# Performance work log

Hardware: AMD Instinct MI355X
Metric: run time of the kernel (lower is better)

## Reference

```python
import jax, jax.numpy as jnp
import numpy as np

N_NODES = 50000
D_FEAT = 512
H1, H2 = 128, 64
N_CLASSES = 40
E_MP = 800000
E_LP = 250000


def gcn_conv(x, W, b, edge_index, edge_weight, num_nodes):
    """PyG GCNConv: add self-loops, symmetric norm D^-1/2 (A+I) D^-1/2, then (norm-agg)(xW)+b."""
    row, col = edge_index[0], edge_index[1]
    loop = jnp.arange(num_nodes)
    row = jnp.concatenate([row, loop])
    col = jnp.concatenate([col, loop])
    ew = jnp.concatenate([edge_weight, jnp.ones((num_nodes,), x.dtype)])
    deg = jax.ops.segment_sum(ew, col, num_segments=num_nodes)
    dinv = jnp.where(deg > 0, deg ** -0.5, 0.0).astype(x.dtype)
    norm = dinv[row] * ew * dinv[col]  # [E+N]
    h = x @ W  # [N, out]
    msg = h[row] * norm[:, None]  # gather + scale per edge
    out = jax.ops.segment_sum(msg, col, num_segments=num_nodes) + b
    return out


def setup_inputs() -> dict:
    key = jax.random.key(0)
    ks = jax.random.split(key, 16)
    inp = {}
    inp["x"] = jax.random.normal(ks[0], (N_NODES, D_FEAT), jnp.float32)
    inp["train_pos_edge_index"] = jax.random.randint(ks[1], (2, E_MP), 0, N_NODES)
    inp["edge_index"] = jax.random.randint(ks[2], (2, E_MP), 0, N_NODES)
    inp["edge_weight"] = jax.random.uniform(ks[3], (E_MP,), jnp.float32)
    inp["pos_edge_index"] = jax.random.randint(ks[4], (2, E_LP), 0, N_NODES)
    inp["neg_edge_index"] = jax.random.randint(ks[5], (2, E_LP), 0, N_NODES)
    # parameters (glorot-ish scaled)
    def w(k, i, o):
        return jax.random.normal(k, (i, o), jnp.float32) * (2.0 / (i + o)) ** 0.5
    inp["W1"] = w(ks[6], D_FEAT, H1)
    inp["b1"] = jnp.zeros((H1,), jnp.float32)
    inp["W2"] = w(ks[7], H1, H2)
    inp["b2"] = jnp.zeros((H2,), jnp.float32)
    inp["W_attr"] = w(ks[8], H2, N_CLASSES)
    inp["b_attr"] = jnp.zeros((N_CLASSES,), jnp.float32)
    inp["W_att"] = w(ks[9], H2, N_CLASSES)
    inp["b_att"] = jnp.zeros((N_CLASSES,), jnp.float32)
    return inp


def reference(x, train_pos_edge_index, edge_index, edge_weight, pos_edge_index,
              neg_edge_index, W1, b1, W2, b2, W_attr, b_attr, W_att, b_att):
    ones = jnp.ones((train_pos_edge_index.shape[1],), x.dtype)
    h = jax.nn.relu(gcn_conv(x, W1, b1, train_pos_edge_index, ones, N_NODES))
    h = gcn_conv(h, W2, b2, train_pos_edge_index, ones, N_NODES)  # [N, 64]
    attr = gcn_conv(h, W_attr, b_attr, edge_index, edge_weight, N_NODES)
    # gradient reversal is identity in forward
    att = gcn_conv(h, W_att, b_att, edge_index, edge_weight, N_NODES)
    total = jnp.concatenate([pos_edge_index, neg_edge_index], axis=-1)  # [2, 2*E_LP]
    x_j = h[total[0]]
    x_i = h[total[1]]
    res = jnp.einsum("ef,ef->e", x_i, x_j)
    return res, jax.nn.log_softmax(attr, axis=1), jax.nn.log_softmax(att, axis=1)
```

## Files before the change

### kernel.cpp

```cpp
#include <hip/hip_runtime.h>

typedef short s16x8 __attribute__((ext_vector_type(8)));
typedef short s16x4 __attribute__((ext_vector_type(4)));
typedef float f32x4 __attribute__((ext_vector_type(4)));

static __device__ __forceinline__ unsigned short f2bf(float f) {
  unsigned u = __float_as_uint(f);
  u += 0x7fff + ((u >> 16) & 1);
  return (unsigned short)(u >> 16);
}
static __device__ __forceinline__ float bf2f(unsigned short h) {
  return __uint_as_float(((unsigned)h) << 16);
}


static __global__ void k_init(int* cntT, int* cntE, int n) {
  int i = blockIdx.x * blockDim.x + threadIdx.x;
  if (i < n) { cntT[i] = 0; cntE[i] = 0; }
}

static __global__ void k_count(const int* __restrict__ tcol, const int* __restrict__ ecol,
                               int* __restrict__ cntT, int* __restrict__ cntE,
                               int* __restrict__ rankT, int* __restrict__ rankE, int E) {
  int e = blockIdx.x * blockDim.x + threadIdx.x;
  if (e < E) {
    rankT[e] = atomicAdd(&cntT[tcol[e]], 1);
    rankE[e] = atomicAdd(&cntE[ecol[e]], 1);
  }
}

static __global__ __launch_bounds__(256) void k_scanA(
    const int* __restrict__ cntT, const int* __restrict__ cntE,
    int* __restrict__ bsum, int n, int nb) {
  const int* cnt = blockIdx.y ? cntE : cntT;
  int tid = threadIdx.x;
  int base = blockIdx.x * 1024 + tid * 4;
  int s = 0;
#pragma unroll
  for (int q = 0; q < 4; ++q) { int i = base + q; if (i < n) s += cnt[i]; }
  __shared__ int red[256];
  red[tid] = s;
  __syncthreads();
  for (int off = 128; off > 0; off >>= 1) {
    if (tid < off) red[tid] += red[tid + off];
    __syncthreads();
  }
  if (tid == 0) bsum[blockIdx.y * nb + blockIdx.x] = red[0];
}

static __global__ void k_scanB(int* bsum, int* ptrT, int* ptrE, int nb, int n) {
  int a = threadIdx.x;
  if (a > 1) return;
  int* bs = bsum + a * nb;
  int run = 0;
  for (int i = 0; i < nb; ++i) { int c = bs[i]; bs[i] = run; run += c; }
  (a ? ptrE : ptrT)[n] = run;
}

static __global__ __launch_bounds__(256) void k_scanC(
    const int* __restrict__ cntT, const int* __restrict__ cntE,
    const int* __restrict__ bsum, int* __restrict__ ptrT, int* __restrict__ ptrE,
    int n, int nb) {
  const int* cnt = blockIdx.y ? cntE : cntT;
  int* ptr = blockIdx.y ? ptrE : ptrT;
  int tid = threadIdx.x;
  int pre = bsum[blockIdx.y * nb + blockIdx.x];
  int base = blockIdx.x * 1024 + tid * 4;
  int v[4];
  int s = 0;
#pragma unroll
  for (int q = 0; q < 4; ++q) { int i = base + q; v[q] = (i < n) ? cnt[i] : 0; s += v[q]; }
  __shared__ int red[256];
  red[tid] = s;
  __syncthreads();
  for (int off = 1; off < 256; off <<= 1) {
    int t = (tid >= off) ? red[tid - off] : 0;
    __syncthreads();
    red[tid] += t;
    __syncthreads();
  }
  int run = pre + (tid ? red[tid - 1] : 0);
#pragma unroll
  for (int q = 0; q < 4; ++q) {
    int i = base + q;
    if (i < n) ptr[i] = run;
    run += v[q];
  }
}

static __global__ void k_fill(const int* __restrict__ trow, const int* __restrict__ tcol,
                              const int* __restrict__ erow, const int* __restrict__ ecol,
                              const float* __restrict__ ew,
                              const int* __restrict__ ptrT, const int* __restrict__ ptrE,
                              const int* __restrict__ rankT, const int* __restrict__ rankE,
                              int* __restrict__ srcT, int2* __restrict__ srcwE, int E) {
  int e = blockIdx.x * blockDim.x + threadIdx.x;
  if (e >= E) return;
  srcT[ptrT[tcol[e]] + rankT[e]] = trow[e];
  int2 p;
  p.x = erow[e];
  p.y = __float_as_int(ew[e]);
  srcwE[ptrE[ecol[e]] + rankE[e]] = p;
}

static __global__ void k_dinv2(const int* __restrict__ cntT, const int2* __restrict__ srcwE,
                               const int* __restrict__ ptrE,
                               float* __restrict__ dinvT, float* __restrict__ dinvE, int n) {
  int i = blockIdx.x * blockDim.x + threadIdx.x;
  if (i >= n) return;
  dinvT[i] = rsqrtf((float)cntT[i] + 1.0f);
  float s = 1.0f;
  int e = ptrE[i + 1];
  for (int j = ptrE[i]; j < e; ++j) s += __int_as_float(srcwE[j].y);
  dinvE[i] = rsqrtf(s);
}


static __global__ void k_cvtW(const float* __restrict__ W, unsigned short* __restrict__ Wh,
                              unsigned short* __restrict__ Wl, int K, int Nc) {
  int t = blockIdx.x * blockDim.x + threadIdx.x;
  if (t >= K * Nc) return;
  int k = t / Nc, c = t - k * Nc;
  float v = W[t];
  unsigned short hi = f2bf(v);
  Wh[(size_t)c * K + k] = hi;
  Wl[(size_t)c * K + k] = f2bf(v - bf2f(hi));
}


#define PADU 36

static __global__ __launch_bounds__(256) void k_gemm_mfma_split(
    const float* __restrict__ A, const unsigned short* __restrict__ Bh,
    const unsigned short* __restrict__ Bl, float* __restrict__ C, int M, int K) {
  __shared__ __align__(16) unsigned short Ah[64][PADU];
  __shared__ __align__(16) unsigned short Al[64][PADU];
  int tid = threadIdx.x;
  int lane = tid & 63, wid = tid >> 6;
  int wr = wid >> 1, wc = wid & 1;
  int l15 = lane & 15, l4 = lane >> 4;
  int brow = blockIdx.x * 64;
  f32x4 acc[2][4] = {};

  float4 v[2];
#pragma unroll
  for (int q = 0; q < 2; ++q) {
    int idx = tid + q * 256;
    int r = idx >> 3, c4 = (idx & 7) * 4;
    int gr = brow + r;
    v[q] = (gr < M) ? *(const float4*)&A[(size_t)gr * K + c4]
                    : make_float4(0.f, 0.f, 0.f, 0.f);
  }

  for (int k0 = 0; k0 < K; k0 += 32) {
    __syncthreads();
#pragma unroll
    for (int q = 0; q < 2; ++q) {
      int idx = tid + q * 256;
      int r = idx >> 3, c4 = (idx & 7) * 4;
      float4 w = v[q];
      unsigned short h0 = f2bf(w.x), h1 = f2bf(w.y), h2 = f2bf(w.z), h3 = f2bf(w.w);
      s16x4 hv = {(short)h0, (short)h1, (short)h2, (short)h3};
      s16x4 lv = {(short)f2bf(w.x - bf2f(h0)), (short)f2bf(w.y - bf2f(h1)),
                  (short)f2bf(w.z - bf2f(h2)), (short)f2bf(w.w - bf2f(h3))};
      *(s16x4*)&Ah[r][c4] = hv;
      *(s16x4*)&Al[r][c4] = lv;
    }
    if (k0 + 32 < K) {
#pragma unroll
      for (int q = 0; q < 2; ++q) {
        int idx = tid + q * 256;
        int r = idx >> 3, c4 = (idx & 7) * 4;
        int gr = brow + r;
        v[q] = (gr < M) ? *(const float4*)&A[(size_t)gr * K + k0 + 32 + c4]
                        : make_float4(0.f, 0.f, 0.f, 0.f);
      }
    }
    __syncthreads();

    s16x8 afh[2], afl[2];
#pragma unroll
    for (int m = 0; m < 2; ++m) {
      int r = wr * 32 + m * 16 + l15;
      afh[m] = *(const s16x8*)&Ah[r][l4 * 8];
      afl[m] = *(const s16x8*)&Al[r][l4 * 8];
    }
    s16x8 bfh[4], bfl[4];
#pragma unroll
    for (int n = 0; n < 4; ++n) {
      int c = wc * 64 + n * 16 + l15;
      bfh[n] = *(const s16x8*)&Bh[(size_t)c * K + k0 + l4 * 8];
      bfl[n] = *(const s16x8*)&Bl[(size_t)c * K + k0 + l4 * 8];
    }
#pragma unroll
    for (int m = 0; m < 2; ++m)
#pragma unroll
      for (int n = 0; n < 4; ++n) {
        acc[m][n] = __builtin_amdgcn_mfma_f32_16x16x32_bf16(afh[m], bfh[n], acc[m][n], 0, 0, 0);
        acc[m][n] = __builtin_amdgcn_mfma_f32_16x16x32_bf16(afl[m], bfh[n], acc[m][n], 0, 0, 0);
        acc[m][n] = __builtin_amdgcn_mfma_f32_16x16x32_bf16(afh[m], bfl[n], acc[m][n], 0, 0, 0);
      }
  }
#pragma unroll
  for (int m = 0; m < 2; ++m) {
    int rbase = brow + wr * 32 + m * 16 + l4 * 4;
#pragma unroll
    for (int n = 0; n < 4; ++n) {
      int c = wc * 64 + n * 16 + l15;
#pragma unroll
      for (int j = 0; j < 4; ++j) {
        int r = rbase + j;
        if (r < M) C[(size_t)r * 128 + c] = acc[m][n][j];
      }
    }
  }
}


template <int F, bool RELU, bool WEIGHTED>
static __global__ __launch_bounds__(256) void k_gather4(
    const float* __restrict__ H, const int* __restrict__ rowptr,
    const int* __restrict__ src, const int2* __restrict__ srcw,
    const float* __restrict__ dinv, const float* __restrict__ Hpre,
    const float* __restrict__ bias, float* __restrict__ out, int n) {
  const int L = F / 4;
  int node = blockIdx.x * (256 / L) + threadIdx.x / L;
  if (node >= n) return;
  int f4 = (threadIdx.x % L) * 4;
  float d = dinv[node];
  float4 hp = *(const float4*)&Hpre[(size_t)node * F + f4];
  float ax = hp.x * d, ay = hp.y * d, az = hp.z * d, aw = hp.w * d;
  int j = rowptr[node], e = rowptr[node + 1];
  for (; j + 1 < e; j += 2) {
    int r0, r1;
    float w0, w1;
    if (WEIGHTED) {
      int2 a = srcw[j], b = srcw[j + 1];
      r0 = a.x; r1 = b.x;
      w0 = dinv[r0] * __int_as_float(a.y);
      w1 = dinv[r1] * __int_as_float(b.y);
    } else {
      r0 = src[j]; r1 = src[j + 1];
      w0 = dinv[r0]; w1 = dinv[r1];
    }
    float4 v0 = *(const float4*)&H[(size_t)r0 * F + f4];
    float4 v1 = *(const float4*)&H[(size_t)r1 * F + f4];
    ax += v0.x * w0 + v1.x * w1;
    ay += v0.y * w0 + v1.y * w1;
    az += v0.z * w0 + v1.z * w1;
    aw += v0.w * w0 + v1.w * w1;
  }
  if (j < e) {
    int r;
    float wj;
    if (WEIGHTED) { int2 a = srcw[j]; r = a.x; wj = dinv[r] * __int_as_float(a.y); }
    else { r = src[j]; wj = dinv[r]; }
    float4 v = *(const float4*)&H[(size_t)r * F + f4];
    ax += v.x * wj; ay += v.y * wj; az += v.z * wj; aw += v.w * wj;
  }
  float bx = 0, by = 0, bz = 0, bw = 0;
  if (bias) { float4 bb = *(const float4*)&bias[f4]; bx = bb.x; by = bb.y; bz = bb.z; bw = bb.w; }
  ax = ax * d + bx; ay = ay * d + by; az = az * d + bz; aw = aw * d + bw;
  if (RELU) { ax = fmaxf(ax, 0.f); ay = fmaxf(ay, 0.f); az = fmaxf(az, 0.f); aw = fmaxf(aw, 0.f); }
  float4 o; o.x = ax; o.y = ay; o.z = az; o.w = aw;
  *(float4*)&out[(size_t)node * F + f4] = o;
}


static __global__ __launch_bounds__(256) void k_gemm(
    const float* __restrict__ A, const float* __restrict__ B,
    const float* __restrict__ bias, float* __restrict__ C,
    int M, int N, int K) {
  const int BM = 64, BN = 64, BK = 16;
  __shared__ float As[BK][BM + 4];
  __shared__ float Bs[BK][BN + 4];
  int tid = threadIdx.x;
  int tr = tid >> 4, tc = tid & 15;
  int brow = blockIdx.y * BM, bcol = blockIdx.x * BN;
  float acc[4][4] = {};
  for (int k0 = 0; k0 < K; k0 += BK) {
#pragma unroll
    for (int i = tid; i < BM * BK; i += 256) {
      int m = i >> 4, kk = i & 15;
      int gr = brow + m;
      As[kk][m] = (gr < M) ? A[(size_t)gr * K + k0 + kk] : 0.f;
    }
#pragma unroll
    for (int i = tid; i < BK * BN; i += 256) {
      int kk = i >> 6, n = i & 63;
      int gc = bcol + n;
      Bs[kk][n] = (gc < N) ? B[(size_t)(k0 + kk) * N + gc] : 0.f;
    }
    __syncthreads();
#pragma unroll
    for (int kk = 0; kk < BK; ++kk) {
      float a[4], b[4];
#pragma unroll
      for (int i = 0; i < 4; ++i) a[i] = As[kk][tr * 4 + i];
#pragma unroll
      for (int j = 0; j < 4; ++j) b[j] = Bs[kk][tc * 4 + j];
#pragma unroll
      for (int i = 0; i < 4; ++i)
#pragma unroll
        for (int j = 0; j < 4; ++j) acc[i][j] += a[i] * b[j];
    }
    __syncthreads();
  }
#pragma unroll
  for (int i = 0; i < 4; ++i) {
    int r = brow + tr * 4 + i;
    if (r >= M) continue;
#pragma unroll
    for (int j = 0; j < 4; ++j) {
      int c = bcol + tc * 4 + j;
      if (c < N) C[(size_t)r * N + c] = acc[i][j] + (bias ? bias[c] : 0.f);
    }
  }
}


static __global__ void k_logsoftmax40(float* __restrict__ X, int n) {
  int i = blockIdx.x * blockDim.x + threadIdx.x;
  if (i >= n) return;
  float4 v[10];
#pragma unroll
  for (int q = 0; q < 10; ++q) v[q] = *(const float4*)&X[(size_t)i * 40 + q * 4];
  float m = -1e30f;
#pragma unroll
  for (int q = 0; q < 10; ++q)
    m = fmaxf(m, fmaxf(fmaxf(v[q].x, v[q].y), fmaxf(v[q].z, v[q].w)));
  float s = 0.f;
#pragma unroll
  for (int q = 0; q < 10; ++q)
    s += expf(v[q].x - m) + expf(v[q].y - m) + expf(v[q].z - m) + expf(v[q].w - m);
  float ls = logf(s) + m;
#pragma unroll
  for (int q = 0; q < 10; ++q) {
    float4 o; o.x = v[q].x - ls; o.y = v[q].y - ls; o.z = v[q].z - ls; o.w = v[q].w - ls;
    *(float4*)&X[(size_t)i * 40 + q * 4] = o;
  }
}


static __global__ __launch_bounds__(256) void k_linkpred4(
    const float* __restrict__ H2, const int* __restrict__ pos,
    const int* __restrict__ neg, float* __restrict__ res, int Elp) {
  int t = blockIdx.x * 256 + threadIdx.x;
  int e = t >> 4, f4 = (t & 15) * 4;
  if (e >= 2 * Elp) return;
  int a, b;
  if (e < Elp) { a = pos[e]; b = pos[Elp + e]; }
  else { int e2 = e - Elp; a = neg[e2]; b = neg[Elp + e2]; }
  float4 va = *(const float4*)&H2[(size_t)a * 64 + f4];
  float4 vb = *(const float4*)&H2[(size_t)b * 64 + f4];
  float p = va.x * vb.x + va.y * vb.y + va.z * vb.z + va.w * vb.w;
  p += __shfl_xor(p, 1);
  p += __shfl_xor(p, 2);
  p += __shfl_xor(p, 4);
  p += __shfl_xor(p, 8);
  if ((t & 15) == 0) res[e] = p;
}


extern "C" void kernel_launch(void* const* d_in, const int* in_sizes, int n_in,
                              void* d_out, int out_size, void* d_ws, size_t ws_size,
                              hipStream_t stream) {
  const float* x    = (const float*)d_in[0];
  const int*   tp   = (const int*)d_in[1];
  const int*   ei   = (const int*)d_in[2];
  const float* ew   = (const float*)d_in[3];
  const int*   pos  = (const int*)d_in[4];
  const int*   neg  = (const int*)d_in[5];
  const float* W1   = (const float*)d_in[6];
  const float* b1   = (const float*)d_in[7];
  const float* W2   = (const float*)d_in[8];
  const float* b2   = (const float*)d_in[9];
  const float* Wattr= (const float*)d_in[10];
  const float* battr= (const float*)d_in[11];
  const float* Watt = (const float*)d_in[12];
  const float* batt = (const float*)d_in[13];

  const int N   = in_sizes[0] / 512;
  const int EMP = in_sizes[1] / 2;
  const int ELP = in_sizes[4] / 2;
  const int NB  = (N + 1023) / 1024;

  float* ws = (float*)d_ws;
  float* dinvT = ws;
  float* dinvE = dinvT + N;
  int* rowptrT = (int*)(dinvE + N);
  int* rowptrE = rowptrT + (N + 4);
  int* srcT    = rowptrE + (N + 4);
  int2* srcwE  = (int2*)(srcT + EMP);
  int* bsum    = (int*)(srcwE + EMP);
  unsigned short* W1h = (unsigned short*)(bsum + 128);
  unsigned short* W1l = W1h + 512 * 128;
  float* bufA  = (float*)(W1l + 512 * 128);
  float* bufB  = bufA + (size_t)N * 128;
  float* bufC  = bufB + (size_t)N * 128;
  int* rankT = (int*)bufA;
  int* rankE = rankT + EMP;
  int* cntT  = (int*)bufB;
  int* cntE  = cntT + N;

  float* out_res  = (float*)d_out;
  float* out_attr = out_res + 2 * (size_t)ELP;
  float* out_att  = out_attr + (size_t)N * 40;

  dim3 b256(256);
  int gN = (N + 255) / 256;
  int gE = (EMP + 255) / 256;

  k_init<<<gN, b256, 0, stream>>>(cntT, cntE, N);
  k_cvtW<<<(512 * 128 + 255) / 256, b256, 0, stream>>>(W1, W1h, W1l, 512, 128);
  k_count<<<gE, b256, 0, stream>>>(tp + EMP, ei + EMP, cntT, cntE, rankT, rankE, EMP);
  {
    dim3 gs(NB, 2);
    k_scanA<<<gs, b256, 0, stream>>>(cntT, cntE, bsum, N, NB);
    k_scanB<<<1, 64, 0, stream>>>(bsum, rowptrT, rowptrE, NB, N);
    k_scanC<<<gs, b256, 0, stream>>>(cntT, cntE, bsum, rowptrT, rowptrE, N, NB);
  }
  k_fill<<<gE, b256, 0, stream>>>(tp, tp + EMP, ei, ei + EMP, ew,
                                  rowptrT, rowptrE, rankT, rankE, srcT, srcwE, EMP);
  k_dinv2<<<gN, b256, 0, stream>>>(cntT, srcwE, rowptrE, dinvT, dinvE, N);

  k_gemm_mfma_split<<<(N + 63) / 64, b256, 0, stream>>>(x, W1h, W1l, bufA, N, 512);
  k_gather4<128, true, false><<<(N + 7) / 8, b256, 0, stream>>>(
      bufA, rowptrT, srcT, nullptr, dinvT, bufA, b1, bufB, N);

  {
    dim3 grid(1, (N + 63) / 64);
    k_gemm<<<grid, b256, 0, stream>>>(bufB, W2, nullptr, bufA, N, 64, 128);
  }
  k_gather4<64, false, false><<<(N + 15) / 16, b256, 0, stream>>>(
      bufA, rowptrT, srcT, nullptr, dinvT, bufA, b2, bufC, N);

  k_gather4<64, false, true><<<(N + 15) / 16, b256, 0, stream>>>(
      bufC, rowptrE, nullptr, srcwE, dinvE, bufC, nullptr, bufA, N);

  {
    dim3 grid(1, (N + 63) / 64);
    k_gemm<<<grid, b256, 0, stream>>>(bufA, Wattr, battr, out_attr, N, 40, 64);
    k_gemm<<<grid, b256, 0, stream>>>(bufA, Watt, batt, out_att, N, 40, 64);
  }
  k_logsoftmax40<<<gN, b256, 0, stream>>>(out_attr, N);
  k_logsoftmax40<<<gN, b256, 0, stream>>>(out_att, N);

  k_linkpred4<<<(2 * ELP * 16 + 255) / 256, b256, 0, stream>>>(bufC, pos, neg, out_res, ELP);
}
```

Measured before the change: 455.6 us.

## Tile W into K-major 32-wide blocks and software-pipeline GEMM B loads

The split-bf16 weight is now stored in 32-element K tiles so each k-step's B fragment sits in one contiguous 8KB chunk. The GEMM main loop is restructured to prefetch the next tile's A rows and B fragments into registers before issuing the current tile's MFMAs, so global load latency overlaps compute. The cost is more live registers for the double-buffered B fragments, which could lower occupancy. The fixed 4096 stride per k-tile assumes 128 output columns.

```diff
diff --git a/kernel.cpp b/kernel.cpp
--- a/kernel.cpp
+++ b/kernel.cpp
@@ -123,8 +123,9 @@
   int k = t / Nc, c = t - k * Nc;
   float v = W[t];
   unsigned short hi = f2bf(v);
-  Wh[(size_t)c * K + k] = hi;
-  Wl[(size_t)c * K + k] = f2bf(v - bf2f(hi));
+  size_t o = (size_t)(k >> 5) * (Nc * 32) + c * 32 + (k & 31);
+  Wh[o] = hi;
+  Wl[o] = f2bf(v - bf2f(hi));
 }
 
 
@@ -140,9 +141,13 @@
   int wr = wid >> 1, wc = wid & 1;
   int l15 = lane & 15, l4 = lane >> 4;
   int brow = blockIdx.x * 64;
+  const int NKT = K >> 5;
   f32x4 acc[2][4] = {};
 
   float4 v[2];
+  s16x8 bhc[4], blc[4], bhn[4], bln[4];
+  s16x8 afh[2], afl[2];
+
 #pragma unroll
   for (int q = 0; q < 2; ++q) {
     int idx = tid + q * 256;
@@ -151,8 +156,60 @@
     v[q] = (gr < M) ? *(const float4*)&A[(size_t)gr * K + c4]
                     : make_float4(0.f, 0.f, 0.f, 0.f);
   }
-
-  for (int k0 = 0; k0 < K; k0 += 32) {
+#pragma unroll
+  for (int n = 0; n < 4; ++n) {
+    size_t o = (size_t)(wc * 64 + n * 16 + l15) * 32 + l4 * 8;
+    bhc[n] = *(const s16x8*)&Bh[o];
+    blc[n] = *(const s16x8*)&Bl[o];
+  }
+#pragma unroll
+  for (int q = 0; q < 2; ++q) {
+    int idx = tid + q * 256;
+    int r = idx >> 3, c4 = (idx & 7) * 4;
+    float4 w = v[q];
+    unsigned short h0 = f2bf(w.x), h1 = f2bf(w.y), h2 = f2bf(w.z), h3 = f2bf(w.w);
+    s16x4 hv = {(short)h0, (short)h1, (short)h2, (short)h3};
+    s16x4 lv = {(short)f2bf(w.x - bf2f(h0)), (short)f2bf(w.y - bf2f(h1)),
+                (short)f2bf(w.z - bf2f(h2)), (short)f2bf(w.w - bf2f(h3))};
+    *(s16x4*)&Ah[r][c4] = hv;
+    *(s16x4*)&Al[r][c4] = lv;
+  }
+  __syncthreads();
+#pragma unroll
+  for (int m = 0; m < 2; ++m) {
+    int r = wr * 32 + m * 16 + l15;
+    afh[m] = *(const s16x8*)&Ah[r][l4 * 8];
+    afl[m] = *(const s16x8*)&Al[r][l4 * 8];
+  }
+
+  for (int kt = 0;; ++kt) {
+    bool more = (kt + 1 < NKT);
+    if (more) {
+      int k0 = (kt + 1) * 32;
+#pragma unroll
+      for (int q = 0; q < 2; ++q) {
+        int idx = tid + q * 256;
+        int r = idx >> 3, c4 = (idx & 7) * 4;
+        int gr = brow + r;
+        v[q] = (gr < M) ? *(const float4*)&A[(size_t)gr * K + k0 + c4]
+                        : make_float4(0.f, 0.f, 0.f, 0.f);
+      }
+#pragma unroll
+      for (int n = 0; n < 4; ++n) {
+        size_t o = (size_t)(kt + 1) * 4096 + (size_t)(wc * 64 + n * 16 + l15) * 32 + l4 * 8;
+        bhn[n] = *(const s16x8*)&Bh[o];
+        bln[n] = *(const s16x8*)&Bl[o];
+      }
+    }
+#pragma unroll
+    for (int m = 0; m < 2; ++m)
+#pragma unroll
+      for (int n = 0; n < 4; ++n) {
+        acc[m][n] = __builtin_amdgcn_mfma_f32_16x16x32_bf16(afh[m], bhc[n], acc[m][n], 0, 0, 0);
+        acc[m][n] = __builtin_amdgcn_mfma_f32_16x16x32_bf16(afl[m], bhc[n], acc[m][n], 0, 0, 0);
+        acc[m][n] = __builtin_amdgcn_mfma_f32_16x16x32_bf16(afh[m], blc[n], acc[m][n], 0, 0, 0);
+      }
+    if (!more) break;
     __syncthreads();
 #pragma unroll
     for (int q = 0; q < 2; ++q) {
@@ -166,41 +223,17 @@
       *(s16x4*)&Ah[r][c4] = hv;
       *(s16x4*)&Al[r][c4] = lv;
     }
-    if (k0 + 32 < K) {
-#pragma unroll
-      for (int q = 0; q < 2; ++q) {
-        int idx = tid + q * 256;
-        int r = idx >> 3, c4 = (idx & 7) * 4;
-        int gr = brow + r;
-        v[q] = (gr < M) ? *(const float4*)&A[(size_t)gr * K + k0 + 32 + c4]
-                        : make_float4(0.f, 0.f, 0.f, 0.f);
-      }
-    }
-    __syncthreads();
-
-    s16x8 afh[2], afl[2];
+    __syncthreads();
 #pragma unroll
     for (int m = 0; m < 2; ++m) {
       int r = wr * 32 + m * 16 + l15;
       afh[m] = *(const s16x8*)&Ah[r][l4 * 8];
       afl[m] = *(const s16x8*)&Al[r][l4 * 8];
     }
-    s16x8 bfh[4], bfl[4];
-#pragma unroll
-    for (int n = 0; n < 4; ++n) {
-      int c = wc * 64 + n * 16 + l15;
-      bfh[n] = *(const s16x8*)&Bh[(size_t)c * K + k0 + l4 * 8];
-      bfl[n] = *(const s16x8*)&Bl[(size_t)c * K + k0 + l4 * 8];
-    }
-#pragma unroll
-    for (int m = 0; m < 2; ++m)
-#pragma unroll
-      for (int n = 0; n < 4; ++n) {
-        acc[m][n] = __builtin_amdgcn_mfma_f32_16x16x32_bf16(afh[m], bfh[n], acc[m][n], 0, 0, 0);
-        acc[m][n] = __builtin_amdgcn_mfma_f32_16x16x32_bf16(afl[m], bfh[n], acc[m][n], 0, 0, 0);
-        acc[m][n] = __builtin_amdgcn_mfma_f32_16x16x32_bf16(afh[m], bfl[n], acc[m][n], 0, 0, 0);
-      }
-  }
+#pragma unroll
+    for (int n = 0; n < 4; ++n) { bhc[n] = bhn[n]; blc[n] = bln[n]; }
+  }
+
 #pragma unroll
   for (int m = 0; m < 2; ++m) {
     int rbase = brow + wr * 32 + m * 16 + l4 * 4;
```

New measurement: 435.0 us. 4.5% less time.

## Double-buffer split-bf16 GEMM, tile W layout, vectorize edge count/fill

Applied to the files above, without the earlier changes.

The first-layer GEMM now double-buffers the A tile in shared memory, prefetches B fragments one k-step ahead in registers, and uses one barrier per k-step. The k-loop is fully unrolled for a fixed K of 512. The converted W1 is stored in a k-tiled layout so each lane's B fragment loads are contiguous, and the edge count and fill kernels each handle four edges per thread with int4 loads. The aim is to hide global load latency behind MFMA work and cut load instruction count, at the cost of more registers and shared memory and of hardcoding K.

```diff
diff --git a/kernel.cpp b/kernel.cpp
--- a/kernel.cpp
+++ b/kernel.cpp
@@ -22,10 +22,26 @@
 static __global__ void k_count(const int* __restrict__ tcol, const int* __restrict__ ecol,
                                int* __restrict__ cntT, int* __restrict__ cntE,
                                int* __restrict__ rankT, int* __restrict__ rankE, int E) {
-  int e = blockIdx.x * blockDim.x + threadIdx.x;
-  if (e < E) {
-    rankT[e] = atomicAdd(&cntT[tcol[e]], 1);
-    rankE[e] = atomicAdd(&cntE[ecol[e]], 1);
+  int base = (blockIdx.x * blockDim.x + threadIdx.x) * 4;
+  if (base + 3 < E) {
+    int4 tc = *(const int4*)&tcol[base];
+    int4 ec = *(const int4*)&ecol[base];
+    int4 rt, re;
+    rt.x = atomicAdd(&cntT[tc.x], 1);
+    rt.y = atomicAdd(&cntT[tc.y], 1);
+    rt.z = atomicAdd(&cntT[tc.z], 1);
+    rt.w = atomicAdd(&cntT[tc.w], 1);
+    re.x = atomicAdd(&cntE[ec.x], 1);
+    re.y = atomicAdd(&cntE[ec.y], 1);
+    re.z = atomicAdd(&cntE[ec.z], 1);
+    re.w = atomicAdd(&cntE[ec.w], 1);
+    *(int4*)&rankT[base] = rt;
+    *(int4*)&rankE[base] = re;
+  } else {
+    for (int e = base; e < E; ++e) {
+      rankT[e] = atomicAdd(&cntT[tcol[e]], 1);
+      rankE[e] = atomicAdd(&cntE[ecol[e]], 1);
+    }
   }
 }
 
@@ -94,13 +110,33 @@
                               const int* __restrict__ ptrT, const int* __restrict__ ptrE,
                               const int* __restrict__ rankT, const int* __restrict__ rankE,
                               int* __restrict__ srcT, int2* __restrict__ srcwE, int E) {
-  int e = blockIdx.x * blockDim.x + threadIdx.x;
-  if (e >= E) return;
-  srcT[ptrT[tcol[e]] + rankT[e]] = trow[e];
-  int2 p;
-  p.x = erow[e];
-  p.y = __float_as_int(ew[e]);
-  srcwE[ptrE[ecol[e]] + rankE[e]] = p;
+  int base = (blockIdx.x * blockDim.x + threadIdx.x) * 4;
+  if (base + 3 < E) {
+    int4 tr = *(const int4*)&trow[base];
+    int4 tc = *(const int4*)&tcol[base];
+    int4 er = *(const int4*)&erow[base];
+    int4 ec = *(const int4*)&ecol[base];
+    float4 w = *(const float4*)&ew[base];
+    int4 rt = *(const int4*)&rankT[base];
+    int4 re = *(const int4*)&rankE[base];
+    srcT[ptrT[tc.x] + rt.x] = tr.x;
+    srcT[ptrT[tc.y] + rt.y] = tr.y;
+    srcT[ptrT[tc.z] + rt.z] = tr.z;
+    srcT[ptrT[tc.w] + rt.w] = tr.w;
+    int2 p;
+    p.x = er.x; p.y = __float_as_int(w.x); srcwE[ptrE[ec.x] + re.x] = p;
+    p.x = er.y; p.y = __float_as_int(w.y); srcwE[ptrE[ec.y] + re.y] = p;
+    p.x = er.z; p.y = __float_as_int(w.z); srcwE[ptrE[ec.z] + re.z] = p;
+    p.x = er.w; p.y = __float_as_int(w.w); srcwE[ptrE[ec.w] + re.w] = p;
+  } else {
+    for (int e = base; e < E; ++e) {
+      srcT[ptrT[tcol[e]] + rankT[e]] = trow[e];
+      int2 p;
+      p.x = erow[e];
+      p.y = __float_as_int(ew[e]);
+      srcwE[ptrE[ecol[e]] + rankE[e]] = p;
+    }
+  }
 }
 
 static __global__ void k_dinv2(const int* __restrict__ cntT, const int2* __restrict__ srcwE,
@@ -123,18 +159,21 @@
   int k = t / Nc, c = t - k * Nc;
   float v = W[t];
   unsigned short hi = f2bf(v);
-  Wh[(size_t)c * K + k] = hi;
-  Wl[(size_t)c * K + k] = f2bf(v - bf2f(hi));
+  size_t o = (size_t)(k >> 5) * (Nc * 32) + c * 32 + (k & 31);
+  Wh[o] = hi;
+  Wl[o] = f2bf(v - bf2f(hi));
 }
 
 
 #define PADU 36
+#define GK 512
+#define NKT 16
 
 static __global__ __launch_bounds__(256) void k_gemm_mfma_split(
     const float* __restrict__ A, const unsigned short* __restrict__ Bh,
-    const unsigned short* __restrict__ Bl, float* __restrict__ C, int M, int K) {
-  __shared__ __align__(16) unsigned short Ah[64][PADU];
-  __shared__ __align__(16) unsigned short Al[64][PADU];
+    const unsigned short* __restrict__ Bl, float* __restrict__ C, int M) {
+  __shared__ __align__(16) unsigned short Ah[2][64][PADU];
+  __shared__ __align__(16) unsigned short Al[2][64][PADU];
   int tid = threadIdx.x;
   int lane = tid & 63, wid = tid >> 6;
   int wr = wid >> 1, wc = wid & 1;
@@ -142,65 +181,103 @@
   int brow = blockIdx.x * 64;
   f32x4 acc[2][4] = {};
 
+  int ar = tid >> 3, ac4 = (tid & 7) * 4;
+  int ar2 = (tid + 256) >> 3, ac42 = ((tid + 256) & 7) * 4;
+  const float* Arow1 = &A[(size_t)min(brow + ar, M - 1) * GK + ac4];
+  const float* Arow2 = &A[(size_t)min(brow + ar2, M - 1) * GK + ac42];
+  bool v1ok = (brow + ar < M), v2ok = (brow + ar2 < M);
+
   float4 v[2];
-#pragma unroll
-  for (int q = 0; q < 2; ++q) {
-    int idx = tid + q * 256;
-    int r = idx >> 3, c4 = (idx & 7) * 4;
-    int gr = brow + r;
-    v[q] = (gr < M) ? *(const float4*)&A[(size_t)gr * K + c4]
-                    : make_float4(0.f, 0.f, 0.f, 0.f);
-  }
-
-  for (int k0 = 0; k0 < K; k0 += 32) {
-    __syncthreads();
-#pragma unroll
-    for (int q = 0; q < 2; ++q) {
-      int idx = tid + q * 256;
-      int r = idx >> 3, c4 = (idx & 7) * 4;
-      float4 w = v[q];
-      unsigned short h0 = f2bf(w.x), h1 = f2bf(w.y), h2 = f2bf(w.z), h3 = f2bf(w.w);
-      s16x4 hv = {(short)h0, (short)h1, (short)h2, (short)h3};
-      s16x4 lv = {(short)f2bf(w.x - bf2f(h0)), (short)f2bf(w.y - bf2f(h1)),
-                  (short)f2bf(w.z - bf2f(h2)), (short)f2bf(w.w - bf2f(h3))};
-      *(s16x4*)&Ah[r][c4] = hv;
-      *(s16x4*)&Al[r][c4] = lv;
-    }
-    if (k0 + 32 < K) {
-#pragma unroll
-      for (int q = 0; q < 2; ++q) {
-        int idx = tid + q * 256;
-        int r = idx >> 3, c4 = (idx & 7) * 4;
-        int gr = brow + r;
-        v[q] = (gr < M) ? *(const float4*)&A[(size_t)gr * K + k0 + 32 + c4]
-                        : make_float4(0.f, 0.f, 0.f, 0.f);
-      }
-    }
-    __syncthreads();
-
+  s16x8 bhc[4], blc[4], bhn[4], bln[4];
+  size_t boff = (size_t)(wc * 64 + l15) * 32 + l4 * 8;
+
+  v[0] = v1ok ? *(const float4*)Arow1 : make_float4(0.f, 0.f, 0.f, 0.f);
+  v[1] = v2ok ? *(const float4*)Arow2 : make_float4(0.f, 0.f, 0.f, 0.f);
+#pragma unroll
+  for (int n = 0; n < 4; ++n) {
+    bhc[n] = *(const s16x8*)&Bh[boff + n * 512];
+    blc[n] = *(const s16x8*)&Bl[boff + n * 512];
+  }
+  {
+    float4 w0 = v[0], w1 = v[1];
+    unsigned short h;
+    s16x4 hv, lv;
+    h = f2bf(w0.x); hv[0] = h; lv[0] = (short)f2bf(w0.x - bf2f(h));
+    h = f2bf(w0.y); hv[1] = h; lv[1] = (short)f2bf(w0.y - bf2f(h));
+    h = f2bf(w0.z); hv[2] = h; lv[2] = (short)f2bf(w0.z - bf2f(h));
+    h = f2bf(w0.w); hv[3] = h; lv[3] = (short)f2bf(w0.w - bf2f(h));
+    *(s16x4*)&Ah[0][ar][ac4] = hv;
+    *(s16x4*)&Al[0][ar][ac4] = lv;
+    h = f2bf(w1.x); hv[0] = h; lv[0] = (short)f2bf(w1.x - bf2f(h));
+    h = f2bf(w1.y); hv[1] = h; lv[1] = (short)f2bf(w1.y - bf2f(h));
+    h = f2bf(w1.z); hv[2] = h; lv[2] = (short)f2bf(w1.z - bf2f(h));
+    h = f2bf(w1.w); hv[3] = h; lv[3] = (short)f2bf(w1.w - bf2f(h));
+    *(s16x4*)&Ah[0][ar2][ac42] = hv;
+    *(s16x4*)&Al[0][ar2][ac42] = lv;
+  }
+  v[0] = v1ok ? *(const float4*)(Arow1 + 32) : make_float4(0.f, 0.f, 0.f, 0.f);
+  v[1] = v2ok ? *(const float4*)(Arow2 + 32) : make_float4(0.f, 0.f, 0.f, 0.f);
+#pragma unroll
+  for (int n = 0; n < 4; ++n) {
+    bhn[n] = *(const s16x8*)&Bh[4096 + boff + n * 512];
+    bln[n] = *(const s16x8*)&Bl[4096 + boff + n * 512];
+  }
+  __syncthreads();
+
+#pragma unroll
+  for (int kt = 0; kt < NKT; ++kt) {
+    int S = kt & 1;
     s16x8 afh[2], afl[2];
 #pragma unroll
     for (int m = 0; m < 2; ++m) {
       int r = wr * 32 + m * 16 + l15;
-      afh[m] = *(const s16x8*)&Ah[r][l4 * 8];
-      afl[m] = *(const s16x8*)&Al[r][l4 * 8];
-    }
-    s16x8 bfh[4], bfl[4];
-#pragma unroll
-    for (int n = 0; n < 4; ++n) {
-      int c = wc * 64 + n * 16 + l15;
-      bfh[n] = *(const s16x8*)&Bh[(size_t)c * K + k0 + l4 * 8];
-      bfl[n] = *(const s16x8*)&Bl[(size_t)c * K + k0 + l4 * 8];
+      afh[m] = *(const s16x8*)&Ah[S][r][l4 * 8];
+      afl[m] = *(const s16x8*)&Al[S][r][l4 * 8];
+    }
+    if (kt + 1 < NKT) {
+      float4 w0 = v[0], w1 = v[1];
+      unsigned short h;
+      s16x4 hv, lv;
+      h = f2bf(w0.x); hv[0] = h; lv[0] = (short)f2bf(w0.x - bf2f(h));
+      h = f2bf(w0.y); hv[1] = h; lv[1] = (short)f2bf(w0.y - bf2f(h));
+      h = f2bf(w0.z); hv[2] = h; lv[2] = (short)f2bf(w0.z - bf2f(h));
+      h = f2bf(w0.w); hv[3] = h; lv[3] = (short)f2bf(w0.w - bf2f(h));
+      *(s16x4*)&Ah[S ^ 1][ar][ac4] = hv;
+      *(s16x4*)&Al[S ^ 1][ar][ac4] = lv;
+      h = f2bf(w1.x); hv[0] = h; lv[0] = (short)f2bf(w1.x - bf2f(h));
+      h = f2bf(w1.y); hv[1] = h; lv[1] = (short)f2bf(w1.y - bf2f(h));
+      h = f2bf(w1.z); hv[2] = h; lv[2] = (short)f2bf(w1.z - bf2f(h));
+      h = f2bf(w1.w); hv[3] = h; lv[3] = (short)f2bf(w1.w - bf2f(h));
+      *(s16x4*)&Ah[S ^ 1][ar2][ac42] = hv;
+      *(s16x4*)&Al[S ^ 1][ar2][ac42] = lv;
+      if (kt + 2 < NKT) {
+        v[0] = v1ok ? *(const float4*)(Arow1 + (kt + 2) * 32) : make_float4(0.f, 0.f, 0.f, 0.f);
+        v[1] = v2ok ? *(const float4*)(Arow2 + (kt + 2) * 32) : make_float4(0.f, 0.f, 0.f, 0.f);
+      }
     }
 #pragma unroll
     for (int m = 0; m < 2; ++m)
 #pragma unroll
       for (int n = 0; n < 4; ++n) {
-        acc[m][n] = __builtin_amdgcn_mfma_f32_16x16x32_bf16(afh[m], bfh[n], acc[m][n], 0, 0, 0);
-        acc[m][n] = __builtin_amdgcn_mfma_f32_16x16x32_bf16(afl[m], bfh[n], acc[m][n], 0, 0, 0);
-        acc[m][n] = __builtin_amdgcn_mfma_f32_16x16x32_bf16(afh[m], bfl[n], acc[m][n], 0, 0, 0);
+        acc[m][n] = __builtin_amdgcn_mfma_f32_16x16x32_bf16(afh[m], bhc[n], acc[m][n], 0, 0, 0);
+        acc[m][n] = __builtin_amdgcn_mfma_f32_16x16x32_bf16(afl[m], bhc[n], acc[m][n], 0, 0, 0);
+        acc[m][n] = __builtin_amdgcn_mfma_f32_16x16x32_bf16(afh[m], blc[n], acc[m][n], 0, 0, 0);
       }
-  }
+    if (kt + 1 < NKT) {
+#pragma unroll
+      for (int n = 0; n < 4; ++n) { bhc[n] = bhn[n]; blc[n] = bln[n]; }
+      if (kt + 2 < NKT) {
+        size_t o = (size_t)(kt + 2) * 4096 + boff;
+#pragma unroll
+        for (int n = 0; n < 4; ++n) {
+          bhn[n] = *(const s16x8*)&Bh[o + n * 512];
+          bln[n] = *(const s16x8*)&Bl[o + n * 512];
+        }
+      }
+      __syncthreads();
+    }
+  }
+
 #pragma unroll
   for (int m = 0; m < 2; ++m) {
     int rbase = brow + wr * 32 + m * 16 + l4 * 4;
@@ -409,22 +486,22 @@
 
   dim3 b256(256);
   int gN = (N + 255) / 256;
-  int gE = (EMP + 255) / 256;
+  int gE4 = (EMP + 1023) / 1024;
 
   k_init<<<gN, b256, 0, stream>>>(cntT, cntE, N);
   k_cvtW<<<(512 * 128 + 255) / 256, b256, 0, stream>>>(W1, W1h, W1l, 512, 128);
-  k_count<<<gE, b256, 0, stream>>>(tp + EMP, ei + EMP, cntT, cntE, rankT, rankE, EMP);
+  k_count<<<gE4, b256, 0, stream>>>(tp + EMP, ei + EMP, cntT, cntE, rankT, rankE, EMP);
   {
     dim3 gs(NB, 2);
     k_scanA<<<gs, b256, 0, stream>>>(cntT, cntE, bsum, N, NB);
     k_scanB<<<1, 64, 0, stream>>>(bsum, rowptrT, rowptrE, NB, N);
     k_scanC<<<gs, b256, 0, stream>>>(cntT, cntE, bsum, rowptrT, rowptrE, N, NB);
   }
-  k_fill<<<gE, b256, 0, stream>>>(tp, tp + EMP, ei, ei + EMP, ew,
-                                  rowptrT, rowptrE, rankT, rankE, srcT, srcwE, EMP);
+  k_fill<<<gE4, b256, 0, stream>>>(tp, tp + EMP, ei, ei + EMP, ew,
+                                   rowptrT, rowptrE, rankT, rankE, srcT, srcwE, EMP);
   k_dinv2<<<gN, b256, 0, stream>>>(cntT, srcwE, rowptrE, dinvT, dinvE, N);
 
-  k_gemm_mfma_split<<<(N + 63) / 64, b256, 0, stream>>>(x, W1h, W1l, bufA, N, 512);
+  k_gemm_mfma_split<<<(N + 63) / 64, b256, 0, stream>>>(x, W1h, W1l, bufA, N);
   k_gather4<128, true, false><<<(N + 7) / 8, b256, 0, stream>>>(
       bufA, rowptrT, srcT, nullptr, dinvT, bufA, b1, bufB, N);
 
```

Measured after the change: 430.4 us. -5.5%, faster.
